# Kernel optimization log

Measured on AMD Instinct MI355X. Metric: run time of the kernel, lower is better.

## Reference

```python
import jax, jax.numpy as jnp
import numpy as np

B, S, E, H = 4, 1024, 1024, 16
D = E // H          # head_dim = 64
F = 4 * E           # mlp inner = 4096
EPS = 1e-5


def _layernorm(x, scale, bias):
    mu = jnp.mean(x, axis=-1, keepdims=True)
    var = jnp.var(x, axis=-1, keepdims=True)
    return (x - mu) * jax.lax.rsqrt(var + EPS) * scale + bias


def setup_inputs() -> dict:
    key = jax.random.key(0)
    ks = jax.random.split(key, 8)
    std = 0.02
    return {
        "hidden_states": jax.random.normal(ks[0], (B, S, E), jnp.float32),
        "ln1_scale": jnp.ones((E,), jnp.float32),
        "ln1_bias": jnp.zeros((E,), jnp.float32),
        # Conv1D kernels stored as (out_features, in_features), applied as x @ k.T
        "w_attn": jax.random.normal(ks[1], (3 * E, E), jnp.float32) * std,
        "b_attn": jnp.zeros((3 * E,), jnp.float32),
        "w_proj": jax.random.normal(ks[2], (E, E), jnp.float32) * std,
        "b_proj": jnp.zeros((E,), jnp.float32),
        "ln2_scale": jnp.ones((E,), jnp.float32),
        "ln2_bias": jnp.zeros((E,), jnp.float32),
        "w_fc": jax.random.normal(ks[3], (F, E), jnp.float32) * std,
        "b_fc": jnp.zeros((F,), jnp.float32),
        "w_proj2": jax.random.normal(ks[4], (E, F), jnp.float32) * std,
        "b_proj2": jnp.zeros((E,), jnp.float32),
    }


def reference(hidden_states, ln1_scale, ln1_bias, w_attn, b_attn, w_proj, b_proj,
              ln2_scale, ln2_bias, w_fc, b_fc, w_proj2, b_proj2):
    x = hidden_states
    # --- attention sub-block ---
    h = _layernorm(x, ln1_scale, ln1_bias)
    qkv = h @ w_attn.T + b_attn                      # [B,S,3E]
    q, k, v = jnp.split(qkv, 3, axis=2)
    q = q.reshape(B, S, H, D) / jnp.sqrt(jnp.float32(D))
    k = k.reshape(B, S, H, D)
    v = v.reshape(B, S, H, D)
    # NOTE: source sets attention_bias = None, so NO causal mask is applied.
    logits = jnp.einsum("bqhd,bkhd->bhqk", q, k)     # [B,H,S,S]
    attn = jax.nn.softmax(logits, axis=-1)
    o = jnp.einsum("bhqk,bkhd->bqhd", attn, v).reshape(B, S, E)
    o = o @ w_proj.T + b_proj
    x = x + o
    # --- mlp sub-block ---
    h = _layernorm(x, ln2_scale, ln2_bias)
    m = jax.nn.gelu(h @ w_fc.T + b_fc, approximate=True)  # gelu_new
    m = m @ w_proj2.T + b_proj2
    return x + m
```

## Files before the change

kernel.cpp:

```cpp
#include <hip/hip_runtime.h>

#define DEV __device__ __forceinline__

using bf16x8 = __attribute__((ext_vector_type(8))) __bf16;
using f32x4  = __attribute__((ext_vector_type(4))) float;
typedef unsigned int u32;
typedef unsigned short u16;
typedef unsigned long long u64;

static constexpr int Bb = 4, Ss = 1024, Ee = 1024, Hh = 16, Dd = 64, Ff = 4096;
static constexpr int Mm = Bb * Ss;

DEV u16 f2bf(float f) {
  union { float f; u32 u; } v; v.f = f;
  u32 r = v.u + 0x7fffu + ((v.u >> 16) & 1u);
  return (u16)(r >> 16);
}

DEV void gload16(const void* g, void* lds) {
  __builtin_amdgcn_global_load_lds(
      (const __attribute__((address_space(1))) void*)(u64)g,
      (__attribute__((address_space(3))) void*)(u32)(u64)lds,
      16, 0, 0);
}

DEV float gelu_tanh(float x) {
  float x3 = x * x * x;
  float t  = tanhf(0.7978845608028654f * (x + 0.044715f * x3));
  return 0.5f * x * (1.0f + t);
}

DEV int swz(int row, int col) { return row * 64 + (col ^ ((row & 7) << 3)); }

DEV f32x4 MFMA(bf16x8 a, bf16x8 b, f32x4 c) {
  return __builtin_amdgcn_mfma_f32_16x16x32_bf16(a, b, c, 0, 0, 0);
}

__global__ __launch_bounds__(256) void cvt_bf16(const float* __restrict__ in,
                                                u16* __restrict__ out, int n) {
  int i = (blockIdx.x * 256 + threadIdx.x) * 8;
  if (i >= n) return;
  float4 a = *(const float4*)(in + i);
  float4 b = *(const float4*)(in + i + 4);
  uint4 o;
  o.x = (u32)f2bf(a.x) | ((u32)f2bf(a.y) << 16);
  o.y = (u32)f2bf(a.z) | ((u32)f2bf(a.w) << 16);
  o.z = (u32)f2bf(b.x) | ((u32)f2bf(b.y) << 16);
  o.w = (u32)f2bf(b.z) | ((u32)f2bf(b.w) << 16);
  *(uint4*)(out + i) = o;
}

__global__ __launch_bounds__(256) void ln_kernel(const float* __restrict__ x,
                                                 const float* __restrict__ scale,
                                                 const float* __restrict__ bias,
                                                 u16* __restrict__ h) {
  const int row = blockIdx.x, tid = threadIdx.x;
  const float4 v = ((const float4*)(x + (size_t)row * Ee))[tid];
  float s  = v.x + v.y + v.z + v.w;
  float ss = v.x * v.x + v.y * v.y + v.z * v.z + v.w * v.w;
  for (int m = 1; m < 64; m <<= 1) {
    s  += __shfl_xor(s, m, 64);
    ss += __shfl_xor(ss, m, 64);
  }
  __shared__ float red[8];
  const int w = tid >> 6, ln = tid & 63;
  if (ln == 0) { red[w * 2] = s; red[w * 2 + 1] = ss; }
  __syncthreads();
  s  = red[0] + red[2] + red[4] + red[6];
  ss = red[1] + red[3] + red[5] + red[7];
  const float mu   = s * (1.0f / Ee);
  const float var  = ss * (1.0f / Ee) - mu * mu;
  const float rstd = rsqrtf(var + 1e-5f);
  const float4 sc = ((const float4*)scale)[tid];
  const float4 bi = ((const float4*)bias)[tid];
  ushort4 o;
  o.x = f2bf((v.x - mu) * rstd * sc.x + bi.x);
  o.y = f2bf((v.y - mu) * rstd * sc.y + bi.y);
  o.z = f2bf((v.z - mu) * rstd * sc.z + bi.z);
  o.w = f2bf((v.w - mu) * rstd * sc.w + bi.w);
  ((ushort4*)(h + (size_t)row * Ee))[tid] = o;
}

template <int EPI, int AM, int AN>
__global__ __launch_bounds__(256, 6) void gemm3(
    const u16* __restrict__ A, const u16* __restrict__ Bw,
    const float* __restrict__ bias, const float* __restrict__ resid,
    float* __restrict__ outf, u16* __restrict__ outb,
    u16* __restrict__ q, u16* __restrict__ k, u16* __restrict__ v,
    int N, int K) {
  constexpr int BM = AM * 32, BN = AN * 32;
  constexpr int GA = BM / 64, GB = BN / 64;
  __shared__ u16 As[2][BM * 32];
  __shared__ u16 Bs[2][BN * 32];
  const int tid = threadIdx.x;
  const int w = tid >> 6, ln = tid & 63;
  const int lr = ln & 15, lg = ln >> 4;
  const int wr = w >> 1, wc = w & 1;

  const int nwg = gridDim.x * gridDim.y;
  const int bid = blockIdx.y * gridDim.x + blockIdx.x;
  const int sid = (bid & 7) * (nwg >> 3) + (bid >> 3);
  const int bx = sid % gridDim.x, by = sid / gridDim.x;
  const int tm = by * BM, tn = bx * BN;

  f32x4 acc[AM][AN];
  f32x4 zero4 = {0.f, 0.f, 0.f, 0.f};
#pragma unroll
  for (int i = 0; i < AM; ++i)
#pragma unroll
    for (int j = 0; j < AN; ++j) acc[i][j] = zero4;

  const int r0 = tid >> 2;
  const int cs = ((tid & 3) ^ (r0 & 3)) * 8;
  const u16* aP[GA];
  const u16* bP[GB];
#pragma unroll
  for (int i = 0; i < GA; ++i) aP[i] = A + (size_t)(tm + r0 + i * 64) * K + cs;
#pragma unroll
  for (int i = 0; i < GB; ++i) bP[i] = Bw + (size_t)(tn + r0 + i * 64) * K + cs;

  auto STAGE = [&](int buf, int k0) {
#pragma unroll
    for (int i = 0; i < GA; ++i)
      gload16(aP[i] + k0, &As[buf][(tid + i * 256) * 8]);
#pragma unroll
    for (int i = 0; i < GB; ++i)
      gload16(bP[i] + k0, &Bs[buf][(tid + i * 256) * 8]);
  };

  const int fsl = (lg ^ (lr & 3)) << 3;
  const int nt = K >> 5;
  STAGE(0, 0);
  asm volatile("s_waitcnt vmcnt(0)" ::: "memory");
  __builtin_amdgcn_s_barrier();

  for (int t = 0; t < nt; ++t) {
    if (t + 1 < nt) STAGE((t + 1) & 1, (t + 1) << 5);
    const u16* Ab = &As[t & 1][0];
    const u16* Bbuf = &Bs[t & 1][0];
    bf16x8 af[AM], bf[AN];
#pragma unroll
    for (int mi = 0; mi < AM; ++mi)
      af[mi] = *(const bf16x8*)&Ab[(wr * AM * 16 + mi * 16 + lr) * 32 + fsl];
#pragma unroll
    for (int ni = 0; ni < AN; ++ni)
      bf[ni] = *(const bf16x8*)&Bbuf[(wc * AN * 16 + ni * 16 + lr) * 32 + fsl];
#pragma unroll
    for (int mi = 0; mi < AM; ++mi)
#pragma unroll
      for (int ni = 0; ni < AN; ++ni)
        acc[mi][ni] = MFMA(af[mi], bf[ni], acc[mi][ni]);
    asm volatile("s_waitcnt vmcnt(0)" ::: "memory");
    __builtin_amdgcn_s_barrier();
  }

#pragma unroll
  for (int mi = 0; mi < AM; ++mi) {
#pragma unroll
    for (int ni = 0; ni < AN; ++ni) {
      const int gc = tn + wc * AN * 16 + ni * 16 + lr;
#pragma unroll
      for (int j = 0; j < 4; ++j) {
        const int gr = tm + wr * AM * 16 + mi * 16 + lg * 4 + j;
        float val = acc[mi][ni][j] + bias[gc];
        if constexpr (EPI == 0) {
          const int which = gc >> 10, hh = (gc >> 6) & 15, dd = gc & 63;
          const int bb2 = gr >> 10, ss2 = gr & 1023;
          const size_t dst = ((size_t)(bb2 * 16 + hh) * 1024 + ss2) * 64 + dd;
          if (which == 0)      q[dst] = f2bf(val * 0.125f);
          else if (which == 1) k[dst] = f2bf(val);
          else                 v[dst] = f2bf(val);
        } else if constexpr (EPI == 1) {
          const size_t idx = (size_t)gr * N + gc;
          outf[idx] = val + resid[idx];
        } else {
          outb[(size_t)gr * N + gc] = f2bf(gelu_tanh(val));
        }
      }
    }
  }
}

__global__ __launch_bounds__(256) void attn3(const u16* __restrict__ qg,
                                             const u16* __restrict__ kg,
                                             const u16* __restrict__ vg,
                                             u16* __restrict__ ao) {
  __shared__ u16 Ks[2][64 * 64];
  __shared__ u16 Vt[2][64 * 64];
  __shared__ u16 Ps[64 * 64];
  const int tid = threadIdx.x;
  const int w = tid >> 6, ln = tid & 63;
  const int lr = ln & 15, lg = ln >> 4;
  const int bh = blockIdx.y;
  const int q0 = blockIdx.x * 64;
  const size_t head = (size_t)bh * (Ss * Dd);

  bf16x8 aq0, aq1;
  {
    const u16* qrow = qg + head + (size_t)(q0 + w * 16 + lr) * Dd;
    aq0 = *(const bf16x8*)(qrow + lg * 8);
    aq1 = *(const bf16x8*)(qrow + 32 + lg * 8);
  }

  const int krow0 = tid >> 3, kg0 = tid & 7;
  const int krow1 = (256 + tid) >> 3, kg1 = tid & 7;
  const int kv0 = tid >> 3;
  const int dsel = tid & 7, d0 = dsel * 8;

  auto KSTORE = [&](int buf, uint4 c0, uint4 c1) {
    *(uint4*)&Ks[buf][krow0 * 64 + ((kg0 ^ (krow0 & 7)) << 3)] = c0;
    *(uint4*)&Ks[buf][krow1 * 64 + ((kg1 ^ (krow1 & 7)) << 3)] = c1;
  };
  auto VSTORE = [&](int buf, uint4 dv, int kv) {
    const u16* pv = (const u16*)&dv;
#pragma unroll
    for (int jj = 0; jj < 8; ++jj) {
      const int j = (jj + dsel) & 7;
      const int dd = d0 + j;
      Vt[buf][dd * 64 + (kv & 7) + (((kv >> 3) ^ (dd & 7)) << 3)] = pv[j];
    }
  };

  {
    const u16* ksrc = kg + head;
    const u16* vsrc = vg + head;
    uint4 kc0 = *(const uint4*)(ksrc + krow0 * 64 + kg0 * 8);
    uint4 kc1 = *(const uint4*)(ksrc + krow1 * 64 + kg1 * 8);
    uint4 va  = *(const uint4*)(vsrc + (size_t)kv0 * Dd + d0);
    uint4 vb  = *(const uint4*)(vsrc + (size_t)(32 + kv0) * Dd + d0);
    KSTORE(0, kc0, kc1);
    VSTORE(0, va, kv0);
    VSTORE(0, vb, 32 + kv0);
  }
  __syncthreads();

  f32x4 zero4 = {0.f, 0.f, 0.f, 0.f};
  f32x4 acc_o[4] = {zero4, zero4, zero4, zero4};
  float mrow[4] = {-1e30f, -1e30f, -1e30f, -1e30f};
  float lrow[4] = {0.f, 0.f, 0.f, 0.f};

  for (int kt = 0; kt < 16; ++kt) {
    const int cur = kt & 1, nc = cur ^ 1;
    const bool more = (kt + 1) < 16;

    uint4 nk0, nk1, nv0, nv1;
    if (more) {
      const u16* knxt = kg + head + (size_t)(kt + 1) * 64 * Dd;
      const u16* vnxt = vg + head + (size_t)(kt + 1) * 64 * Dd;
      nk0 = *(const uint4*)(knxt + krow0 * 64 + kg0 * 8);
      nk1 = *(const uint4*)(knxt + krow1 * 64 + kg1 * 8);
      nv0 = *(const uint4*)(vnxt + (size_t)kv0 * Dd + d0);
      nv1 = *(const uint4*)(vnxt + (size_t)(32 + kv0) * Dd + d0);
    }

    f32x4 sa[4];
#pragma unroll
    for (int kf = 0; kf < 4; ++kf) {
      bf16x8 bk0 = *(const bf16x8*)&Ks[cur][swz(kf * 16 + lr, lg * 8)];
      bf16x8 bk1 = *(const bf16x8*)&Ks[cur][swz(kf * 16 + lr, 32 + lg * 8)];
      f32x4 s = zero4;
      s = MFMA(aq0, bk0, s);
      s = MFMA(aq1, bk1, s);
      sa[kf] = s;
    }

#pragma unroll
    for (int j = 0; j < 4; ++j) {
      float mx = fmaxf(fmaxf(sa[0][j], sa[1][j]), fmaxf(sa[2][j], sa[3][j]));
      mx = fmaxf(mx, __shfl_xor(mx, 1, 64));
      mx = fmaxf(mx, __shfl_xor(mx, 2, 64));
      mx = fmaxf(mx, __shfl_xor(mx, 4, 64));
      mx = fmaxf(mx, __shfl_xor(mx, 8, 64));
      const float nm = fmaxf(mrow[j], mx);
      const float corr = __expf(mrow[j] - nm);
      mrow[j] = nm;
      float ssum = 0.f;
#pragma unroll
      for (int kf = 0; kf < 4; ++kf) {
        const float p = __expf(sa[kf][j] - nm);
        sa[kf][j] = p;
        ssum += p;
      }
      ssum += __shfl_xor(ssum, 1, 64);
      ssum += __shfl_xor(ssum, 2, 64);
      ssum += __shfl_xor(ssum, 4, 64);
      ssum += __shfl_xor(ssum, 8, 64);
      lrow[j] = lrow[j] * corr + ssum;
#pragma unroll
      for (int df = 0; df < 4; ++df) acc_o[df][j] *= corr;
    }

#pragma unroll
    for (int kf = 0; kf < 4; ++kf)
#pragma unroll
      for (int j = 0; j < 4; ++j)
        Ps[swz(w * 16 + lg * 4 + j, kf * 16 + lr)] = f2bf(sa[kf][j]);

    __syncthreads();

    bf16x8 ap0 = *(const bf16x8*)&Ps[swz(w * 16 + lr, lg * 8)];
    bf16x8 ap1 = *(const bf16x8*)&Ps[swz(w * 16 + lr, 32 + lg * 8)];
#pragma unroll
    for (int df = 0; df < 4; ++df) {
      bf16x8 bv0 = *(const bf16x8*)&Vt[cur][swz(df * 16 + lr, lg * 8)];
      bf16x8 bv1 = *(const bf16x8*)&Vt[cur][swz(df * 16 + lr, 32 + lg * 8)];
      acc_o[df] = MFMA(ap0, bv0, acc_o[df]);
      acc_o[df] = MFMA(ap1, bv1, acc_o[df]);
    }

    if (more) {
      KSTORE(nc, nk0, nk1);
      VSTORE(nc, nv0, kv0);
      VSTORE(nc, nv1, 32 + kv0);
    }
    __syncthreads();
  }

  const int b = bh >> 4, h = bh & 15;
#pragma unroll
  for (int df = 0; df < 4; ++df) {
#pragma unroll
    for (int j = 0; j < 4; ++j) {
      const int srow = q0 + w * 16 + lg * 4 + j;
      const int e = h * 64 + df * 16 + lr;
      ao[((size_t)b * Ss + srow) * Ee + e] = f2bf(acc_o[df][j] / lrow[j]);
    }
  }
}

extern "C" void kernel_launch(void* const* d_in, const int* in_sizes, int n_in,
                              void* d_out, int out_size, void* d_ws, size_t ws_size,
                              hipStream_t stream) {
  const float* x      = (const float*)d_in[0];
  const float* ln1_s  = (const float*)d_in[1];
  const float* ln1_b  = (const float*)d_in[2];
  const float* w_attn = (const float*)d_in[3];
  const float* b_attn = (const float*)d_in[4];
  const float* w_proj = (const float*)d_in[5];
  const float* b_proj = (const float*)d_in[6];
  const float* ln2_s  = (const float*)d_in[7];
  const float* ln2_b  = (const float*)d_in[8];
  const float* w_fc   = (const float*)d_in[9];
  const float* b_fc   = (const float*)d_in[10];
  const float* w_proj2= (const float*)d_in[11];
  const float* b_proj2= (const float*)d_in[12];
  float* out = (float*)d_out;

  char* base = (char*)d_ws;
  size_t off = 0;
  auto alloc = [&](size_t bytes) { char* p = base + off; off += bytes; return p; };
  u16* wA   = (u16*)alloc((size_t)3 * Ee * Ee * 2);
  u16* wP   = (u16*)alloc((size_t)Ee * Ee * 2);
  u16* wF   = (u16*)alloc((size_t)Ff * Ee * 2);
  u16* wP2  = (u16*)alloc((size_t)Ee * Ff * 2);
  u16* h1   = (u16*)alloc((size_t)Mm * Ee * 2);
  u16* qws  = (u16*)alloc((size_t)Mm * Ee * 2);
  u16* kws  = (u16*)alloc((size_t)Mm * Ee * 2);
  u16* vws  = (u16*)alloc((size_t)Mm * Ee * 2);
  u16* aws  = (u16*)alloc((size_t)Mm * Ee * 2);
  float* x1 = (float*)alloc((size_t)Mm * Ee * 4);
  u16* mfc  = qws;

  cvt_bf16<<<3 * Ee * Ee / 2048, 256, 0, stream>>>(w_attn, wA, 3 * Ee * Ee);
  cvt_bf16<<<Ee * Ee / 2048, 256, 0, stream>>>(w_proj, wP, Ee * Ee);
  cvt_bf16<<<Ff * Ee / 2048, 256, 0, stream>>>(w_fc, wF, Ff * Ee);
  cvt_bf16<<<Ee * Ff / 2048, 256, 0, stream>>>(w_proj2, wP2, Ee * Ff);

  ln_kernel<<<Mm, 256, 0, stream>>>(x, ln1_s, ln1_b, h1);
  gemm3<0, 4, 2><<<dim3(48, 32), 256, 0, stream>>>(h1, wA, b_attn, nullptr,
                                                   nullptr, nullptr, qws, kws, vws,
                                                   3 * Ee, Ee);
  attn3<<<dim3(16, 64), 256, 0, stream>>>(qws, kws, vws, aws);
  gemm3<1, 2, 2><<<dim3(16, 64), 256, 0, stream>>>(aws, wP, b_proj, x,
                                                   x1, nullptr, nullptr, nullptr, nullptr,
                                                   Ee, Ee);
  ln_kernel<<<Mm, 256, 0, stream>>>(x1, ln2_s, ln2_b, h1);
  gemm3<2, 4, 2><<<dim3(64, 32), 256, 0, stream>>>(h1, wF, b_fc, nullptr,
                                                   nullptr, mfc, nullptr, nullptr, nullptr,
                                                   Ff, Ee);
  gemm3<1, 2, 2><<<dim3(16, 64), 256, 0, stream>>>(mfc, wP2, b_proj2, x1,
                                                   out, nullptr, nullptr, nullptr, nullptr,
                                                   Ee, Ff);
}
```

Baseline: 315.3 us.

## Load K tiles via global_load_lds, remap attention blocks, retile final projection GEMM

```diff
diff --git a/kernel.cpp b/kernel.cpp
--- a/kernel.cpp
+++ b/kernel.cpp
@@ -181,7 +181,7 @@
   }
 }
 
-__global__ __launch_bounds__(256) void attn3(const u16* __restrict__ qg,
+__global__ __launch_bounds__(256) void attn5(const u16* __restrict__ qg,
                                              const u16* __restrict__ kg,
                                              const u16* __restrict__ vg,
                                              u16* __restrict__ ao) {
@@ -191,8 +191,10 @@
   const int tid = threadIdx.x;
   const int w = tid >> 6, ln = tid & 63;
   const int lr = ln & 15, lg = ln >> 4;
-  const int bh = blockIdx.y;
-  const int q0 = blockIdx.x * 64;
+
+  const int bid = blockIdx.x;
+  const int bh = (bid & 7) * 8 + ((bid >> 3) & 7);
+  const int q0 = (bid >> 6) * 64;
   const size_t head = (size_t)bh * (Ss * Dd);
 
   bf16x8 aq0, aq1;
@@ -202,15 +204,16 @@
     aq1 = *(const bf16x8*)(qrow + 32 + lg * 8);
   }
 
-  const int krow0 = tid >> 3, kg0 = tid & 7;
-  const int krow1 = (256 + tid) >> 3, kg1 = tid & 7;
+  const int kr0 = tid >> 3,        ks0 = (tid & 7) ^ (kr0 & 7);
+  const int kr1 = (256 + tid) >> 3, ks1 = (tid & 7) ^ (kr1 & 7);
+  auto GLOADK = [&](int buf, int kt) {
+    const u16* base = kg + head + (size_t)kt * 4096;
+    gload16(base + kr0 * 64 + ks0 * 8, &Ks[buf][tid * 8]);
+    gload16(base + kr1 * 64 + ks1 * 8, &Ks[buf][(256 + tid) * 8]);
+  };
+
   const int kv0 = tid >> 3;
   const int dsel = tid & 7, d0 = dsel * 8;
-
-  auto KSTORE = [&](int buf, uint4 c0, uint4 c1) {
-    *(uint4*)&Ks[buf][krow0 * 64 + ((kg0 ^ (krow0 & 7)) << 3)] = c0;
-    *(uint4*)&Ks[buf][krow1 * 64 + ((kg1 ^ (krow1 & 7)) << 3)] = c1;
-  };
   auto VSTORE = [&](int buf, uint4 dv, int kv) {
     const u16* pv = (const u16*)&dv;
 #pragma unroll
@@ -222,17 +225,15 @@
   };
 
   {
-    const u16* ksrc = kg + head;
+    GLOADK(0, 0);
     const u16* vsrc = vg + head;
-    uint4 kc0 = *(const uint4*)(ksrc + krow0 * 64 + kg0 * 8);
-    uint4 kc1 = *(const uint4*)(ksrc + krow1 * 64 + kg1 * 8);
-    uint4 va  = *(const uint4*)(vsrc + (size_t)kv0 * Dd + d0);
-    uint4 vb  = *(const uint4*)(vsrc + (size_t)(32 + kv0) * Dd + d0);
-    KSTORE(0, kc0, kc1);
+    uint4 va = *(const uint4*)(vsrc + (size_t)kv0 * Dd + d0);
+    uint4 vb = *(const uint4*)(vsrc + (size_t)(32 + kv0) * Dd + d0);
     VSTORE(0, va, kv0);
     VSTORE(0, vb, 32 + kv0);
-  }
-  __syncthreads();
+    asm volatile("s_waitcnt vmcnt(0)" ::: "memory");
+    __builtin_amdgcn_s_barrier();
+  }
 
   f32x4 zero4 = {0.f, 0.f, 0.f, 0.f};
   f32x4 acc_o[4] = {zero4, zero4, zero4, zero4};
@@ -243,12 +244,10 @@
     const int cur = kt & 1, nc = cur ^ 1;
     const bool more = (kt + 1) < 16;
 
-    uint4 nk0, nk1, nv0, nv1;
+    uint4 nv0, nv1;
     if (more) {
-      const u16* knxt = kg + head + (size_t)(kt + 1) * 64 * Dd;
-      const u16* vnxt = vg + head + (size_t)(kt + 1) * 64 * Dd;
-      nk0 = *(const uint4*)(knxt + krow0 * 64 + kg0 * 8);
-      nk1 = *(const uint4*)(knxt + krow1 * 64 + kg1 * 8);
+      GLOADK(nc, kt + 1);
+      const u16* vnxt = vg + head + (size_t)(kt + 1) * 4096;
       nv0 = *(const uint4*)(vnxt + (size_t)kv0 * Dd + d0);
       nv1 = *(const uint4*)(vnxt + (size_t)(32 + kv0) * Dd + d0);
     }
@@ -309,11 +308,11 @@
     }
 
     if (more) {
-      KSTORE(nc, nk0, nk1);
       VSTORE(nc, nv0, kv0);
       VSTORE(nc, nv1, 32 + kv0);
-    }
-    __syncthreads();
+      asm volatile("s_waitcnt vmcnt(0)" ::: "memory");
+      __syncthreads();
+    }
   }
 
   const int b = bh >> 4, h = bh & 15;
@@ -370,7 +369,7 @@
   gemm3<0, 4, 2><<<dim3(48, 32), 256, 0, stream>>>(h1, wA, b_attn, nullptr,
                                                    nullptr, nullptr, qws, kws, vws,
                                                    3 * Ee, Ee);
-  attn3<<<dim3(16, 64), 256, 0, stream>>>(qws, kws, vws, aws);
+  attn5<<<1024, 256, 0, stream>>>(qws, kws, vws, aws);
   gemm3<1, 2, 2><<<dim3(16, 64), 256, 0, stream>>>(aws, wP, b_proj, x,
                                                    x1, nullptr, nullptr, nullptr, nullptr,
                                                    Ee, Ee);
@@ -378,7 +377,7 @@
   gemm3<2, 4, 2><<<dim3(64, 32), 256, 0, stream>>>(h1, wF, b_fc, nullptr,
                                                    nullptr, mfc, nullptr, nullptr, nullptr,
                                                    Ff, Ee);
-  gemm3<1, 2, 2><<<dim3(16, 64), 256, 0, stream>>>(mfc, wP2, b_proj2, x1,
+  gemm3<1, 4, 2><<<dim3(16, 32), 256, 0, stream>>>(mfc, wP2, b_proj2, x1,
                                                    out, nullptr, nullptr, nullptr, nullptr,
                                                    Ee, Ff);
 }
```

Result: no change. 311.0 us (-1.4%).
